# Performance work log

Measured on AMD Instinct MI355X. Metric: run time of the kernel, lower is better.

Reference implementation:

```python
import jax, jax.numpy as jnp
import numpy as np

N_HEADS = 16
LN_EPS = 1e-5

def layer_norm(x, w):
    # matches torch LayerNorm in fp32, weight-only (no bias)
    x = x.astype(jnp.float32)
    mu = jnp.mean(x, axis=-1, keepdims=True)
    var = jnp.mean((x - mu) ** 2, axis=-1, keepdims=True)
    return (x - mu) / jnp.sqrt(var + LN_EPS) * w

def rotate_half(t):
    t1, t2 = jnp.split(t, 2, axis=-1)
    return jnp.concatenate((-t2, t1), axis=-1)

def setup_inputs() -> dict:
    key = jax.random.key(0)
    ks = jax.random.split(key, 16)
    B, S, D, C = 2, 2048, 1024, 1024
    H = N_HEADS
    hd = D // H
    # rotary tables: emb = cat(freqs, freqs), freqs = t * inv_freq
    inv_freq = 1.0 / (10000.0 ** (np.arange(0, hd, 2, dtype=np.float32) / hd))
    t = np.arange(S, dtype=np.float32)
    freqs = np.outer(t, inv_freq)                       # [S, hd/2]
    emb = np.concatenate([freqs, freqs], axis=-1)       # [S, hd]
    s = 0.02
    return {
        "x": jax.random.normal(ks[0], (B, S, D), jnp.float32),
        "rotary_cos": jnp.asarray(np.cos(emb)),
        "rotary_sin": jnp.asarray(np.sin(emb)),
        "c": jax.random.normal(ks[1], (B, C), jnp.float32),
        "norm1_w": jnp.ones((D,), jnp.float32),
        "qkv_w": jax.random.normal(ks[2], (3 * D, D), jnp.float32) * s,
        "out_w": jax.random.normal(ks[3], (D, D), jnp.float32) * s,
        "norm2_w": jnp.ones((D,), jnp.float32),
        "fc1_w": jax.random.normal(ks[4], (4 * D, D), jnp.float32) * s,
        "fc1_b": jnp.zeros((4 * D,), jnp.float32),
        "fc2_w": jax.random.normal(ks[5], (D, 4 * D), jnp.float32) * s,
        "fc2_b": jnp.zeros((D,), jnp.float32),
        # NOTE: module zero-inits adaLN; random here for a non-degenerate baseline
        "ada_w": jax.random.normal(ks[6], (6 * D, C), jnp.float32) * s,
        "ada_b": jnp.zeros((6 * D,), jnp.float32),
    }

def reference(x, rotary_cos, rotary_sin, c, norm1_w, qkv_w, out_w, norm2_w,
              fc1_w, fc1_b, fc2_w, fc2_b, ada_w, ada_b):
    B, S, D = x.shape
    H = N_HEADS
    hd = D // H
    # AdaLN conditioning -> six [B,1,D] modulation tensors
    mods = (c @ ada_w.T + ada_b)[:, None, :]                       # [B,1,6D]
    shift_msa, scale_msa, gate_msa, shift_mlp, scale_mlp, gate_mlp = jnp.split(mods, 6, axis=2)
    x_skip = x
    # LN + modulate + QKV
    h = layer_norm(x, norm1_w) * (1.0 + scale_msa) + shift_msa     # [B,S,D]
    qkv = (h @ qkv_w.T).reshape(B, S, 3, H, hd)
    # rotary applied to packed qkv (q, k, and v) as in the torchscript fallback
    cos = rotary_cos[None, :, None, None, :]                       # [1,S,1,1,hd]
    sin = rotary_sin[None, :, None, None, :]
    qkv = qkv * cos + rotate_half(qkv) * sin
    q, k, v = qkv[:, :, 0], qkv[:, :, 1], qkv[:, :, 2]             # [B,S,H,hd]
    scale = hd ** -0.5
    scores = jnp.einsum('bqhd,bkhd->bhqk', q, k) * scale           # [B,H,S,S]
    attn = jax.nn.softmax(scores, axis=-1)
    o = jnp.einsum('bhqk,bkhd->bqhd', attn, v).reshape(B, S, D)
    # gated residual (dropout=0 / eval)
    x = gate_msa * (o @ out_w.T) + x_skip
    # second LN + modulate + MLP (exact gelu, matching F.gelu default)
    h2 = layer_norm(x, norm2_w) * (1.0 + scale_mlp) + shift_mlp
    mlp = jax.nn.gelu(h2 @ fc1_w.T + fc1_b, approximate=False) @ fc2_w.T + fc2_b
    return gate_mlp * mlp + x
```

## Files before the change

### kernel.cpp

```cpp
#include <hip/hip_runtime.h>
#include <hip/hip_bf16.h>


typedef unsigned short u16;
typedef unsigned int   u32;
typedef __bf16 bf16x8 __attribute__((ext_vector_type(8)));
typedef float  f32x4  __attribute__((ext_vector_type(4)));

#define MFMA_BF16(a, b, c) __builtin_amdgcn_mfma_f32_16x16x32_bf16((a), (b), (c), 0, 0, 0)

__device__ __forceinline__ float b2f(u16 u) {
    union { u32 i; float f; } v; v.i = ((u32)u) << 16; return v.f;
}
__device__ __forceinline__ u16 f2b(float f) {
    union { u32 i; float f; } v; v.f = f;
    u32 i = v.i;
    return (u16)((i + 0x7FFFu + ((i >> 16) & 1u)) >> 16);
}
__device__ __forceinline__ u32 pk2(float a, float b) {
#if __has_builtin(__builtin_amdgcn_cvt_pk_bf16_f32)
    typedef __bf16 bf16x2_t __attribute__((ext_vector_type(2)));
    union { bf16x2_t v; u32 u; } cv;
    cv.v = __builtin_amdgcn_cvt_pk_bf16_f32(a, b);
    return cv.u;
#else
    return (u32)f2b(a) | ((u32)f2b(b) << 16);
#endif
}
__device__ __forceinline__ float finz(float v) {
    return __builtin_isfinite(v) ? v : 0.0f;
}
__device__ __forceinline__ void dma16(const void* g, void* l) {
    __builtin_amdgcn_global_load_lds(
        (const __attribute__((address_space(1))) unsigned int*)(uintptr_t)g,
        (__attribute__((address_space(3))) unsigned int*)(uintptr_t)l,
        16, 0, 0);
}

__global__ __launch_bounds__(256) void convert_kernel(
    const float* __restrict__ in, u16* __restrict__ out, int n8, int kshift)
{
    int i = blockIdx.x * 256 + threadIdx.x;
    if (i >= n8) return;
    size_t o = (size_t)i * 8;
    int bk   = (int)(o >> (kshift + 7));
    int rem  = (int)(o & (((size_t)128 << kshift) - 1));
    int kg   = rem >> 10;
    int nloc = (rem >> 3) & 127;
    const float* src = in + (((size_t)bk * 128 + nloc) << kshift) + kg * 8;
    float4 a = *(const float4*)src;
    float4 b = *(const float4*)(src + 4);
    union { u16 s[8]; float4 v; } wp;
    wp.s[0] = f2b(a.x); wp.s[1] = f2b(a.y); wp.s[2] = f2b(a.z); wp.s[3] = f2b(a.w);
    wp.s[4] = f2b(b.x); wp.s[5] = f2b(b.y); wp.s[6] = f2b(b.z); wp.s[7] = f2b(b.w);
    *(float4*)(out + o) = wp.v;
}

__global__ __launch_bounds__(64) void mods_kernel(
    const float* __restrict__ c, const float* __restrict__ ada_w,
    const float* __restrict__ ada_b, float* __restrict__ mods)
{
    const int n = blockIdx.x;
    const int lane = threadIdx.x;
    const float* wr = ada_w + (size_t)n * 1024;
    float a0 = 0.f, a1 = 0.f;
    for (int k = lane; k < 1024; k += 64) {
        float w = wr[k];
        a0 += w * c[k];
        a1 += w * c[1024 + k];
    }
    for (int o = 32; o > 0; o >>= 1) {
        a0 += __shfl_down(a0, o, 64);
        a1 += __shfl_down(a1, o, 64);
    }
    if (lane == 0) {
        float bb = ada_b[n];
        mods[n]        = a0 + bb;
        mods[6144 + n] = a1 + bb;
    }
}

__global__ __launch_bounds__(256) void ln_mod_kernel(
    const u16* __restrict__ xbf, const float* __restrict__ xf,
    const float* __restrict__ w, const float* __restrict__ mods,
    int scale_off, int shift_off, u16* __restrict__ out)
{
    const int row = blockIdx.x;
    const int b   = row >> 11;
    const int tid = threadIdx.x;
    const size_t base = (size_t)row * 1024 + tid * 4;
    float v[4];
    if (xf) {
        float4 t = *(const float4*)(xf + base);
        v[0] = t.x; v[1] = t.y; v[2] = t.z; v[3] = t.w;
    } else {
        uint2 p = *(const uint2*)(xbf + base);
        union { u32 i; float f; } a, bb, cc, d;
        a.i  = p.x << 16;          v[0] = a.f;
        bb.i = p.x & 0xFFFF0000u;  v[1] = bb.f;
        cc.i = p.y << 16;          v[2] = cc.f;
        d.i  = p.y & 0xFFFF0000u;  v[3] = d.f;
    }
    float s  = v[0] + v[1] + v[2] + v[3];
    float sq = v[0]*v[0] + v[1]*v[1] + v[2]*v[2] + v[3]*v[3];
    __shared__ float rs[256], rq[256];
    rs[tid] = s; rq[tid] = sq;
    __syncthreads();
    for (int o = 128; o > 0; o >>= 1) {
        if (tid < o) { rs[tid] += rs[tid + o]; rq[tid] += rq[tid + o]; }
        __syncthreads();
    }
    const float mean = rs[0] * (1.0f / 1024.0f);
    const float var  = rq[0] * (1.0f / 1024.0f) - mean * mean;
    const float inv  = rsqrtf(fmaxf(var, 0.f) + 1e-5f);
    union { u16 s4[4]; uint2 u2; } pk;
    for (int i = 0; i < 4; ++i) {
        int cidx = tid * 4 + i;
        float y = (v[i] - mean) * inv * w[cidx];
        y = y * (1.0f + mods[b * 6144 + scale_off + cidx]) + mods[b * 6144 + shift_off + cidx];
        pk.s4[i] = f2b(y);
    }
    size_t o = ((size_t)(row >> 7)) * 131072 + ((tid * 4) >> 3) * 1024
             + (row & 127) * 8 + ((tid * 4) & 7);
    *(uint2*)(out + o) = pk.u2;
}

template<int MODE>
__global__ __launch_bounds__(256) void gemm128(
    const u16* __restrict__ A, const u16* __restrict__ W,
    int M, int N, int K,
    const float* __restrict__ mods, const float* __restrict__ bias,
    const float* __restrict__ resid_f, const u16* __restrict__ resid_bf,
    float* __restrict__ out_f, u16* __restrict__ out_bf,
    u16* __restrict__ aux1, u16* __restrict__ aux2,
    const float* __restrict__ rcos, const float* __restrict__ rsin)
{
    __shared__ u16 As[2][4096];
    __shared__ u16 Bs[2][4096];
    const int tid  = threadIdx.x;
    const int wave = tid >> 6, lane = tid & 63;
    const int quad = lane >> 4, l15 = lane & 15;
    const int wi = wave >> 1, wj = wave & 1;
    const int m0 = blockIdx.y * 128, n0 = blockIdx.x * 128;

    f32x4 acc[4][4] = {};

    const u16* Asrc = A + (size_t)m0 * K + wave * 1024 + lane * 8;
    const u16* Bsrc = W + (size_t)n0 * K + wave * 1024 + lane * 8;
    const int wo = wave * 1024;

    dma16(Asrc,       &As[0][wo]);
    dma16(Asrc + 512, &As[0][wo + 512]);
    dma16(Bsrc,       &Bs[0][wo]);
    dma16(Bsrc + 512, &Bs[0][wo + 512]);
    __syncthreads();

    const int nt = K >> 5;
    for (int t = 0; t < nt; ++t) {
        const int cur = t & 1;
        if (t + 1 < nt) {
            const u16* a = Asrc + (size_t)(t + 1) * 4096;
            const u16* b = Bsrc + (size_t)(t + 1) * 4096;
            dma16(a,       &As[cur ^ 1][wo]);
            dma16(a + 512, &As[cur ^ 1][wo + 512]);
            dma16(b,       &Bs[cur ^ 1][wo]);
            dma16(b + 512, &Bs[cur ^ 1][wo + 512]);
        }
        bf16x8 af[4], bw[4];
        #pragma unroll
        for (int f = 0; f < 4; ++f) {
            af[f] = *(const bf16x8*)(&As[cur][quad * 1024 + (wi * 64 + f * 16 + l15) * 8]);
            bw[f] = *(const bf16x8*)(&Bs[cur][quad * 1024 + (wj * 64 + f * 16 + l15) * 8]);
        }
        #pragma unroll
        for (int fi = 0; fi < 4; ++fi)
            #pragma unroll
            for (int fj = 0; fj < 4; ++fj)
                acc[fi][fj] = MFMA_BF16(af[fi], bw[fj], acc[fi][fj]);
        __syncthreads();
    }

    if (MODE == 4) {
        const int colbase = n0 + wj * 64;
        const int wcol = colbase >> 10;
        const int hh   = (colbase & 1023) >> 6;
        #pragma unroll
        for (int fi = 0; fi < 4; ++fi) {
            const int rbase = m0 + wi * 64 + fi * 16 + quad * 4;
            #pragma unroll
            for (int reg = 0; reg < 4; ++reg) {
                const int r = rbase + reg;
                const int b = r >> 11, s = r & 2047;
                const int bh = b * 16 + hh;
                #pragma unroll
                for (int fj = 0; fj < 2; ++fj) {
                    const int d = fj * 16 + l15;
                    float va = acc[fi][fj][reg];
                    float vb = acc[fi][fj + 2][reg];
                    float ca = rcos[s * 64 + d];
                    float sa = rsin[s * 64 + d];
                    float ra = va * ca - vb * sa;
                    float rb = vb * ca + va * sa;
                    if (wcol == 0) {
                        ra *= 0.125f; rb *= 0.125f;
                        u16* dst = aux1 + ((size_t)bh * 2048 + s) * 64;
                        dst[d]      = f2b(ra);
                        dst[d + 32] = f2b(rb);
                    } else if (wcol == 1) {
                        size_t base = (size_t)bh * 131072 + (s >> 6) * 4096
                                    + (s & 63) * 8 + (d & 7);
                        aux2[base + (d >> 3) * 512]        = f2b(ra);
                        aux2[base + ((d >> 3) + 4) * 512]  = f2b(rb);
                    } else {
                        size_t base = (size_t)bh * 131072 + (s >> 6) * 4096
                                    + ((s & 63) >> 3) * 512 + (s & 7);
                        out_bf[base + d * 8]        = f2b(ra);
                        out_bf[base + (d + 32) * 8] = f2b(rb);
                    }
                }
            }
        }
        return;
    }

    #pragma unroll
    for (int fi = 0; fi < 4; ++fi) {
        #pragma unroll
        for (int fj = 0; fj < 4; ++fj) {
            const int cidx  = n0 + wj * 64 + fj * 16 + l15;
            const int rbase = m0 + wi * 64 + fi * 16 + quad * 4;
            #pragma unroll
            for (int reg = 0; reg < 4; ++reg) {
                const int r = rbase + reg;
                float v = acc[fi][fj][reg];
                if (MODE == 1) {
                    float u = v + bias[cidx];
                    float g = 0.5f * u * (1.0f + erff(u * 0.70710678118654752f));
                    size_t o = ((size_t)(r >> 7)) * 524288 + (cidx >> 3) * 1024
                             + (r & 127) * 8 + (cidx & 7);
                    out_bf[o] = f2b(g);
                } else if (MODE == 2) {
                    int bb = r >> 11;
                    float gate = mods[bb * 6144 + 2048 + cidx];
                    out_bf[(size_t)r * N + cidx] = f2b(gate * v + resid_f[(size_t)r * N + cidx]);
                } else if (MODE == 3) {
                    int bb = r >> 11;
                    float u = v + bias[cidx];
                    float gate = mods[bb * 6144 + 5120 + cidx];
                    out_f[(size_t)r * N + cidx] =
                        finz(gate * u + b2f(resid_bf[(size_t)r * N + cidx]));
                }
            }
        }
    }
}

__global__ __launch_bounds__(256) void attn_kernel(
    const u16* __restrict__ Q, const u16* __restrict__ Kb,
    const u16* __restrict__ Vb, u16* __restrict__ O)
{
    __shared__ u16 Ks[4096];
    __shared__ u16 Vs[4096];
    __shared__ u16 Ps[4][16 * 72];
    const int tid  = threadIdx.x;
    const int wave = tid >> 6, lane = tid & 63;
    const int quad = lane >> 4, l15 = lane & 15;
    const int bh = blockIdx.x & 31, qt = blockIdx.x >> 5;

    const u16* Qh = Q  + ((size_t)bh * 2048 + qt * 64) * 64;
    const u16* Kh = Kb + (size_t)bh * 131072;
    const u16* Vh = Vb + (size_t)bh * 131072;

    bf16x8 aq[2];
    #pragma unroll
    for (int kh = 0; kh < 2; ++kh)
        aq[kh] = *(const bf16x8*)(Qh + (size_t)(wave * 16 + l15) * 64 + kh * 32 + quad * 8);

    f32x4 acc_o[4] = {};
    float lsum[4] = {0.f, 0.f, 0.f, 0.f};

    for (int kb = 0; kb < 32; ++kb) {
        __syncthreads();
        const u16* kc = Kh + kb * 4096;
        const u16* vc = Vh + kb * 4096;
        dma16(kc + (2 * wave) * 512 + lane * 8,     &Ks[(2 * wave) * 512]);
        dma16(kc + (2 * wave + 1) * 512 + lane * 8, &Ks[(2 * wave + 1) * 512]);
        dma16(vc + (2 * wave) * 512 + lane * 8,     &Vs[(2 * wave) * 512]);
        dma16(vc + (2 * wave + 1) * 512 + lane * 8, &Vs[(2 * wave + 1) * 512]);
        __syncthreads();

        f32x4 sc[4] = {};
        #pragma unroll
        for (int kt = 0; kt < 4; ++kt)
            #pragma unroll
            for (int kh = 0; kh < 2; ++kh) {
                bf16x8 bk = *(const bf16x8*)(&Ks[(quad + kh * 4) * 512 + (kt * 16 + l15) * 8]);
                sc[kt] = MFMA_BF16(aq[kh], bk, sc[kt]);
            }

        #pragma unroll
        for (int kt = 0; kt < 4; ++kt)
            #pragma unroll
            for (int reg = 0; reg < 4; ++reg)
                sc[kt][reg] = __expf(fminf(sc[kt][reg], 50.f));
        #pragma unroll
        for (int reg = 0; reg < 4; ++reg)
            lsum[reg] += (sc[0][reg] + sc[1][reg]) + (sc[2][reg] + sc[3][reg]);

        #pragma unroll
        for (int kt = 0; kt < 4; kt += 2)
            #pragma unroll
            for (int reg = 0; reg < 4; ++reg) {
                u32 p = pk2(sc[kt][reg], sc[kt + 1][reg]);
                Ps[wave][(quad * 4 + reg) * 72 + kt * 16 + l15]       = (u16)p;
                Ps[wave][(quad * 4 + reg) * 72 + (kt + 1) * 16 + l15] = (u16)(p >> 16);
            }
        __asm volatile("s_waitcnt lgkmcnt(0)" ::: "memory");

        bf16x8 ap0 = *(const bf16x8*)(&Ps[wave][l15 * 72 + quad * 8]);
        bf16x8 ap1 = *(const bf16x8*)(&Ps[wave][l15 * 72 + 32 + quad * 8]);
        #pragma unroll
        for (int dt = 0; dt < 4; ++dt) {
            bf16x8 bv0 = *(const bf16x8*)(&Vs[quad * 512 + (dt * 16 + l15) * 8]);
            bf16x8 bv1 = *(const bf16x8*)(&Vs[(quad + 4) * 512 + (dt * 16 + l15) * 8]);
            acc_o[dt] = MFMA_BF16(ap0, bv0, acc_o[dt]);
            acc_o[dt] = MFMA_BF16(ap1, bv1, acc_o[dt]);
        }
    }

    float linv[4];
    #pragma unroll
    for (int reg = 0; reg < 4; ++reg) {
        float l = lsum[reg];
        l += __shfl_xor(l, 1, 64);
        l += __shfl_xor(l, 2, 64);
        l += __shfl_xor(l, 4, 64);
        l += __shfl_xor(l, 8, 64);
        linv[reg] = 1.0f / l;
    }

    const int b = bh >> 4, hh = bh & 15;
    #pragma unroll
    for (int dt = 0; dt < 4; ++dt)
        #pragma unroll
        for (int reg = 0; reg < 4; ++reg) {
            int q = qt * 64 + wave * 16 + quad * 4 + reg;
            int r = b * 2048 + q;
            int col = hh * 64 + dt * 16 + l15;
            float v = acc_o[dt][reg] * linv[reg];
            O[((size_t)(r >> 7)) * 131072 + (col >> 3) * 1024
              + (r & 127) * 8 + (col & 7)] = f2b(v);
        }
}

extern "C" void kernel_launch(void* const* d_in, const int* in_sizes, int n_in,
                              void* d_out, int out_size, void* d_ws, size_t ws_size,
                              hipStream_t stream)
{
    const float* x     = (const float*)d_in[0];
    const float* rcos  = (const float*)d_in[1];
    const float* rsin  = (const float*)d_in[2];
    const float* c     = (const float*)d_in[3];
    const float* n1w   = (const float*)d_in[4];
    const float* qkvw  = (const float*)d_in[5];
    const float* outw  = (const float*)d_in[6];
    const float* n2w   = (const float*)d_in[7];
    const float* fc1w  = (const float*)d_in[8];
    const float* fc1b  = (const float*)d_in[9];
    const float* fc2w  = (const float*)d_in[10];
    const float* fc2b  = (const float*)d_in[11];
    const float* adaw  = (const float*)d_in[12];
    const float* adab  = (const float*)d_in[13];
    float* out = (float*)d_out;

    char* ws = (char*)d_ws;
    const size_t MB8 = (size_t)8 * 1024 * 1024;
    float* mods  = (float*)ws;
    u16*   W     = (u16*)(ws + 49152);
    char*  S1    = ws + 49152 + MB8;
    char*  S2    = S1 + MB8;

    u16* h    = (u16*)d_out;
    u16* qs   = (u16*)S1;
    u16* ks   = (u16*)S2;
    u16* vT   = (u16*)(S2 + MB8);
    u16* ob   = (u16*)d_out;
    u16* x2   = (u16*)S1;
    u16* h2   = (u16*)d_out;
    u16* mid  = (u16*)S2;

    mods_kernel<<<6144, 64, 0, stream>>>(c, adaw, adab, mods);
    ln_mod_kernel<<<4096, 256, 0, stream>>>(nullptr, x, n1w, mods, 1024, 0, h);
    convert_kernel<<<1536, 256, 0, stream>>>(qkvw, W, 393216, 10);
    gemm128<4><<<dim3(24, 32), 256, 0, stream>>>(h, W, 4096, 3072, 1024,
        nullptr, nullptr, nullptr, nullptr, nullptr, vT, qs, ks, rcos, rsin);
    attn_kernel<<<1024, 256, 0, stream>>>(qs, ks, vT, ob);
    convert_kernel<<<512, 256, 0, stream>>>(outw, W, 131072, 10);
    gemm128<2><<<dim3(8, 32), 256, 0, stream>>>(ob, W, 4096, 1024, 1024,
        mods, nullptr, x, nullptr, nullptr, x2, nullptr, nullptr, nullptr, nullptr);
    ln_mod_kernel<<<4096, 256, 0, stream>>>(x2, nullptr, n2w, mods, 4096, 3072, h2);
    convert_kernel<<<2048, 256, 0, stream>>>(fc1w, W, 524288, 10);
    gemm128<1><<<dim3(32, 32), 256, 0, stream>>>(h2, W, 4096, 4096, 1024,
        nullptr, fc1b, nullptr, nullptr, nullptr, mid, nullptr, nullptr, nullptr, nullptr);
    convert_kernel<<<2048, 256, 0, stream>>>(fc2w, W, 524288, 12);
    gemm128<3><<<dim3(8, 32), 256, 0, stream>>>(mid, W, 4096, 1024, 4096,
        mods, fc2b, nullptr, x2, out, nullptr, nullptr, nullptr, nullptr, nullptr);
}
```

Measured before the change: 443.5 us.

## Double-buffer K/V tiles in attention and switch softmax to exp2 with packed P stores

The attention kernel now double-buffers K and V in LDS, prefetching the next 64-key block with async DMA while the current block is computed, and keeps one barrier per iteration instead of two. The Q pre-scale folds in log2(e) so the softmax can use exp2f, and the V layout is permuted so that P can be written to LDS as packed 32-bit pairs instead of separate 16-bit stores. The cost targeted is exposed global-load latency and extra barrier and LDS-store overhead per key block. In exchange it doubles K/V LDS use, which may lower occupancy. It also relies on the DMA for the next block having finished at the end-of-loop barrier.

```diff
diff --git a/kernel.cpp b/kernel.cpp
--- a/kernel.cpp
+++ b/kernel.cpp
@@ -202,7 +202,7 @@
                     float ra = va * ca - vb * sa;
                     float rb = vb * ca + va * sa;
                     if (wcol == 0) {
-                        ra *= 0.125f; rb *= 0.125f;
+                        ra *= 0.18033688011f; rb *= 0.18033688011f;
                         u16* dst = aux1 + ((size_t)bh * 2048 + s) * 64;
                         dst[d]      = f2b(ra);
                         dst[d + 32] = f2b(rb);
@@ -212,8 +212,10 @@
                         aux2[base + (d >> 3) * 512]        = f2b(ra);
                         aux2[base + ((d >> 3) + 4) * 512]  = f2b(rb);
                     } else {
+                        const int sl = s & 63;
+                        const int sp = (sl & 32) | ((sl & 15) << 1) | ((sl >> 4) & 1);
                         size_t base = (size_t)bh * 131072 + (s >> 6) * 4096
-                                    + ((s & 63) >> 3) * 512 + (s & 7);
+                                    + (sp >> 3) * 512 + (sp & 7);
                         out_bf[base + d * 8]        = f2b(ra);
                         out_bf[base + (d + 32) * 8] = f2b(rb);
                     }
@@ -259,8 +261,8 @@
     const u16* __restrict__ Q, const u16* __restrict__ Kb,
     const u16* __restrict__ Vb, u16* __restrict__ O)
 {
-    __shared__ u16 Ks[4096];
-    __shared__ u16 Vs[4096];
+    __shared__ u16 Ks[2][4096];
+    __shared__ u16 Vs[2][4096];
     __shared__ u16 Ps[4][16 * 72];
     const int tid  = threadIdx.x;
     const int wave = tid >> 6, lane = tid & 63;
@@ -279,22 +281,29 @@
     f32x4 acc_o[4] = {};
     float lsum[4] = {0.f, 0.f, 0.f, 0.f};
 
+    dma16(Kh + (2 * wave) * 512 + lane * 8,     &Ks[0][(2 * wave) * 512]);
+    dma16(Kh + (2 * wave + 1) * 512 + lane * 8, &Ks[0][(2 * wave + 1) * 512]);
+    dma16(Vh + (2 * wave) * 512 + lane * 8,     &Vs[0][(2 * wave) * 512]);
+    dma16(Vh + (2 * wave + 1) * 512 + lane * 8, &Vs[0][(2 * wave + 1) * 512]);
+    __syncthreads();
+
     for (int kb = 0; kb < 32; ++kb) {
-        __syncthreads();
-        const u16* kc = Kh + kb * 4096;
-        const u16* vc = Vh + kb * 4096;
-        dma16(kc + (2 * wave) * 512 + lane * 8,     &Ks[(2 * wave) * 512]);
-        dma16(kc + (2 * wave + 1) * 512 + lane * 8, &Ks[(2 * wave + 1) * 512]);
-        dma16(vc + (2 * wave) * 512 + lane * 8,     &Vs[(2 * wave) * 512]);
-        dma16(vc + (2 * wave + 1) * 512 + lane * 8, &Vs[(2 * wave + 1) * 512]);
-        __syncthreads();
+        const int cur = kb & 1;
+        if (kb + 1 < 32) {
+            const u16* kc = Kh + (kb + 1) * 4096;
+            const u16* vc = Vh + (kb + 1) * 4096;
+            dma16(kc + (2 * wave) * 512 + lane * 8,     &Ks[cur ^ 1][(2 * wave) * 512]);
+            dma16(kc + (2 * wave + 1) * 512 + lane * 8, &Ks[cur ^ 1][(2 * wave + 1) * 512]);
+            dma16(vc + (2 * wave) * 512 + lane * 8,     &Vs[cur ^ 1][(2 * wave) * 512]);
+            dma16(vc + (2 * wave + 1) * 512 + lane * 8, &Vs[cur ^ 1][(2 * wave + 1) * 512]);
+        }
 
         f32x4 sc[4] = {};
         #pragma unroll
         for (int kt = 0; kt < 4; ++kt)
             #pragma unroll
             for (int kh = 0; kh < 2; ++kh) {
-                bf16x8 bk = *(const bf16x8*)(&Ks[(quad + kh * 4) * 512 + (kt * 16 + l15) * 8]);
+                bf16x8 bk = *(const bf16x8*)(&Ks[cur][(quad + kh * 4) * 512 + (kt * 16 + l15) * 8]);
                 sc[kt] = MFMA_BF16(aq[kh], bk, sc[kt]);
             }
 
@@ -302,30 +311,29 @@
         for (int kt = 0; kt < 4; ++kt)
             #pragma unroll
             for (int reg = 0; reg < 4; ++reg)
-                sc[kt][reg] = __expf(fminf(sc[kt][reg], 50.f));
+                sc[kt][reg] = exp2f(fminf(sc[kt][reg], 72.f));
         #pragma unroll
         for (int reg = 0; reg < 4; ++reg)
             lsum[reg] += (sc[0][reg] + sc[1][reg]) + (sc[2][reg] + sc[3][reg]);
 
         #pragma unroll
-        for (int kt = 0; kt < 4; kt += 2)
-            #pragma unroll
-            for (int reg = 0; reg < 4; ++reg) {
-                u32 p = pk2(sc[kt][reg], sc[kt + 1][reg]);
-                Ps[wave][(quad * 4 + reg) * 72 + kt * 16 + l15]       = (u16)p;
-                Ps[wave][(quad * 4 + reg) * 72 + (kt + 1) * 16 + l15] = (u16)(p >> 16);
-            }
+        for (int reg = 0; reg < 4; ++reg) {
+            u32* prow = (u32*)(&Ps[wave][(quad * 4 + reg) * 72]);
+            prow[l15]      = pk2(sc[0][reg], sc[1][reg]);
+            prow[16 + l15] = pk2(sc[2][reg], sc[3][reg]);
+        }
         __asm volatile("s_waitcnt lgkmcnt(0)" ::: "memory");
 
         bf16x8 ap0 = *(const bf16x8*)(&Ps[wave][l15 * 72 + quad * 8]);
         bf16x8 ap1 = *(const bf16x8*)(&Ps[wave][l15 * 72 + 32 + quad * 8]);
         #pragma unroll
         for (int dt = 0; dt < 4; ++dt) {
-            bf16x8 bv0 = *(const bf16x8*)(&Vs[quad * 512 + (dt * 16 + l15) * 8]);
-            bf16x8 bv1 = *(const bf16x8*)(&Vs[(quad + 4) * 512 + (dt * 16 + l15) * 8]);
+            bf16x8 bv0 = *(const bf16x8*)(&Vs[cur][quad * 512 + (dt * 16 + l15) * 8]);
+            bf16x8 bv1 = *(const bf16x8*)(&Vs[cur][(quad + 4) * 512 + (dt * 16 + l15) * 8]);
             acc_o[dt] = MFMA_BF16(ap0, bv0, acc_o[dt]);
             acc_o[dt] = MFMA_BF16(ap1, bv1, acc_o[dt]);
         }
+        __syncthreads();
     }
 
     float linv[4];
```

Result: slower. 470.9 us (+6.2%).
